# Kernel optimization log

Hardware: AMD Instinct MI355X
Metric: run time of the kernel (lower is better)

## Reference

```python
import jax, jax.numpy as jnp
import numpy as np

N_NODES = 100000
N_EDGES = 1600000
IN_DIM = 128
HID = 128
OUT = 64


def gcn_conv(x, src, dst, W, b, n_nodes):
    # x: [N, Din] -> [N, Dout]; symmetric-normalized GCN with self-loops (PyG GCNConv defaults)
    h = x @ W  # transform first (as PyG does)
    loop = jnp.arange(n_nodes, dtype=src.dtype)
    s = jnp.concatenate([src, loop])
    d = jnp.concatenate([dst, loop])
    deg = jax.ops.segment_sum(jnp.ones_like(d, dtype=h.dtype), d, num_segments=n_nodes)
    dis = jnp.where(deg > 0, jax.lax.rsqrt(deg), 0.0)
    norm = dis[s] * dis[d]  # [E+N]
    msgs = h[s] * norm[:, None]  # gather-transform
    out = jax.ops.segment_sum(msgs, d, num_segments=n_nodes)  # scatter-add
    return out + b


def setup_inputs() -> dict:
    key = jax.random.key(0)
    ks = jax.random.split(key, 12)
    x = jax.random.normal(ks[0], (N_NODES, IN_DIM), dtype=jnp.float32)
    edge_index = jax.random.randint(ks[1], (2, N_EDGES), 0, N_NODES, dtype=jnp.int32)
    def lin(k, fan_in, fan_out):
        bound = 1.0 / np.sqrt(fan_in)
        kw, kb = jax.random.split(k)
        W = jax.random.uniform(kw, (fan_in, fan_out), minval=-bound, maxval=bound, dtype=jnp.float32)
        b = jax.random.uniform(kb, (fan_out,), minval=-bound, maxval=bound, dtype=jnp.float32)
        return W, b
    W1, b1 = lin(ks[2], IN_DIM, HID)
    W2, b2 = lin(ks[3], HID, HID)
    Wp1, bp1 = lin(ks[4], HID, HID)
    Wp2, bp2 = lin(ks[5], HID, OUT)
    return {"x": x, "edge_index": edge_index,
            "W1": W1, "b1": b1, "W2": W2, "b2": b2,
            "Wp1": Wp1, "bp1": bp1, "Wp2": Wp2, "bp2": bp2}


def reference(x, edge_index, W1, b1, W2, b2, Wp1, bp1, Wp2, bp2):
    n = x.shape[0]
    src, dst = edge_index[0], edge_index[1]
    # layer 1: GCNConv + relu (dropout inactive at eval)
    h = jax.nn.relu(gcn_conv(x, src, dst, W1, b1, n))
    # layer 2
    h = jax.nn.relu(gcn_conv(h, src, dst, W2, b2, n))
    # post MLP head
    h = h @ Wp1 + bp1
    h = h @ Wp2 + bp2
    return jax.nn.log_softmax(h, axis=1)
```

## Files before the change

kernel.cpp:

```cpp
#include <hip/hip_runtime.h>
#include <hip/hip_bf16.h>
#include <cstdint>

typedef __attribute__((ext_vector_type(8))) short short8;
typedef __attribute__((ext_vector_type(16))) float f32x16;
typedef unsigned short us;

#define BIN_SHIFT 9
#define BIN_NODES 512
#define CAPB 12288
#define EPB 4096

__device__ __forceinline__ float bflo(uint32_t u) { return __builtin_bit_cast(float, u << 16); }
__device__ __forceinline__ float bfhi(uint32_t u) { return __builtin_bit_cast(float, u & 0xffff0000u); }

__device__ __forceinline__ us f32_to_bf16_rne(float f) {
  uint32_t u = __builtin_bit_cast(uint32_t, f);
  u += 0x7fffu + ((u >> 16) & 1u);
  return (us)(u >> 16);
}

__device__ __forceinline__ void split2(float f, us& h, us& l) {
  uint32_t u = __builtin_bit_cast(uint32_t, f);
  h = (us)(u >> 16);
  float fh = __builtin_bit_cast(float, u & 0xffff0000u);
  float r = f - fh;
  l = (us)(__builtin_bit_cast(uint32_t, r) >> 16);
}

__global__ __launch_bounds__(256) void k_binA(
    const int* __restrict__ src, const int* __restrict__ dst,
    uint2* __restrict__ binbuf, int* __restrict__ gcur, int E, int nbins) {
  __shared__ uint2 stage[EPB];
  __shared__ int cnt[256], base[256], cur[256], gbase[256];
  int tid = threadIdx.x;
  int e0 = blockIdx.x * EPB;
  int ne = min(EPB, E - e0);
  if (ne <= 0) return;
  cnt[tid] = 0;
  __syncthreads();
  for (int i = tid; i < ne; i += 256) atomicAdd(&cnt[dst[e0 + i] >> BIN_SHIFT], 1);
  __syncthreads();
  if (tid < 64) {
    int carry = 0;
#pragma unroll
    for (int c = 0; c < 4; ++c) {
      int v = cnt[c * 64 + tid];
      int incl = v;
#pragma unroll
      for (int off = 1; off < 64; off <<= 1) {
        int t = __shfl_up(incl, off, 64);
        if (tid >= off) incl += t;
      }
      base[c * 64 + tid] = carry + incl - v;
      carry += __shfl(incl, 63, 64);
    }
  }
  __syncthreads();
  if (tid < nbins && cnt[tid] > 0) gbase[tid] = atomicAdd(&gcur[tid], cnt[tid]);
  cur[tid] = base[tid];
  __syncthreads();
  for (int i = tid; i < ne; i += 256) {
    int d = dst[e0 + i], s = src[e0 + i];
    int p = atomicAdd(&cur[d >> BIN_SHIFT], 1);
    stage[p] = make_uint2((unsigned)d, (unsigned)s);
  }
  __syncthreads();
  for (int i = tid; i < ne; i += 256) {
    uint2 en = stage[i];
    int b = en.x >> BIN_SHIFT;
    int gi = gbase[b] + (i - base[b]);
    if (gi < CAPB) binbuf[(size_t)b * CAPB + gi] = en;
  }
}

__global__ __launch_bounds__(256) void k_passB(
    const uint2* __restrict__ binbuf, const int* __restrict__ gcur,
    int* __restrict__ deg, float* __restrict__ dis, int* __restrict__ start,
    int* __restrict__ col, int N, int nbins) {
  __shared__ int hist[512], lstart[512], cur[512];
  __shared__ int colstage[CAPB];
  __shared__ int binbase_s;
  int b = blockIdx.x, tid = threadIdx.x;
  int node0 = b << BIN_SHIFT;
  int cnt = min(gcur[b], CAPB);
  hist[tid] = 0; hist[tid + 256] = 0;
  __syncthreads();
  const uint2* bp = binbuf + (size_t)b * CAPB;
  for (int i = tid; i < cnt; i += 256) atomicAdd(&hist[bp[i].x & (BIN_NODES - 1)], 1);
  __syncthreads();
  if (tid < 64) {
    int s = 0;
    for (int i = tid; i < b; i += 64) s += min(gcur[i], CAPB);
#pragma unroll
    for (int off = 32; off; off >>= 1) s += __shfl_xor(s, off, 64);
    if (tid == 0) binbase_s = s;
    int carry = 0;
#pragma unroll
    for (int c = 0; c < 8; ++c) {
      int v = hist[c * 64 + tid];
      int incl = v;
#pragma unroll
      for (int off = 1; off < 64; off <<= 1) {
        int t = __shfl_up(incl, off, 64);
        if (tid >= off) incl += t;
      }
      lstart[c * 64 + tid] = carry + incl - v;
      carry += __shfl(incl, 63, 64);
    }
  }
  __syncthreads();
  int binbase = binbase_s;
  for (int i = tid; i < 512; i += 256) {
    int node = node0 + i;
    if (node < N) {
      int dg = hist[i];
      deg[node] = dg;
      dis[node] = rsqrtf((float)(dg + 1));
      start[node] = binbase + lstart[i];
    }
  }
  cur[tid] = lstart[tid]; cur[tid + 256] = lstart[tid + 256];
  __syncthreads();
  for (int i = tid; i < cnt; i += 256) {
    uint2 en = bp[i];
    int p = atomicAdd(&cur[en.x & (BIN_NODES - 1)], 1);
    colstage[p] = (int)en.y;
  }
  __syncthreads();
  for (int i = tid; i < cnt; i += 256) col[binbase + i] = colstage[i];
}

__global__ void k_prep(const float* __restrict__ W1, const float* __restrict__ W2,
                       const float* __restrict__ Wp1, const float* __restrict__ Wp2,
                       const float* __restrict__ bp1, const float* __restrict__ bp2,
                       us* __restrict__ Wt1h, us* __restrict__ Wt1l,
                       us* __restrict__ Wt2h, us* __restrict__ Wt2l,
                       us* __restrict__ Wch, us* __restrict__ Wcl, float* __restrict__ bc) {
  int blk = blockIdx.x, tid = threadIdx.x;
  if (blk < 128) {
    const float* W = (blk < 64) ? W1 : W2;
    us* Wh = (blk < 64) ? Wt1h : Wt2h;
    us* Wl = (blk < 64) ? Wt1l : Wt2l;
    int idx = (blk & 63) * 256 + tid;
    int k = idx >> 7, n = idx & 127;
    us h, l;
    split2(W[idx], h, l);
    Wh[n * 128 + k] = h;
    Wl[n * 128 + k] = l;
  } else if (blk < 160) {
    int idx = (blk - 128) * 256 + tid;
    int k = idx >> 6, j = idx & 63;
    float acc = 0.f;
    for (int t = 0; t < 128; ++t) acc += Wp1[k * 128 + t] * Wp2[t * 64 + j];
    us h, l;
    split2(acc, h, l);
    Wch[j * 128 + k] = h;
    Wcl[j * 128 + k] = l;
  } else {
    int j = tid;
    if (j < 64) {
      float acc = bp2[j];
      for (int t = 0; t < 128; ++t) acc += bp1[t] * Wp2[t * 64 + j];
      bc[j] = acc;
    }
  }
}

template <bool AF32>
__global__ __launch_bounds__(256) void k_gemm_mfma(
    const void* __restrict__ Av, const us* __restrict__ Wh,
    const us* __restrict__ Wl, const float* __restrict__ dis,
    us* __restrict__ out_bf16, int N, int ntiles) {
  __shared__ us As_hi[32 * 136];
  __shared__ us As_lo[32 * 136];
  int tid = threadIdx.x;
  int wave = tid >> 6, lane = tid & 63;
  int n0 = wave * 32;
  int nn = n0 + (lane & 31);
  int khalf = (lane >> 5) * 8;
  int m = lane & 31;

  short8 bh[8], bl[8];
#pragma unroll
  for (int c = 0; c < 8; ++c) {
    bh[c] = *(const short8*)&Wh[nn * 128 + c * 16 + khalf];
    bl[c] = *(const short8*)&Wl[nn * 128 + c * 16 + khalf];
  }

  for (int t = blockIdx.x; t < ntiles; t += gridDim.x) {
    int row0 = t * 32;
    __syncthreads();
    if (AF32) {
      const float* A = (const float*)Av;
      for (int j = tid; j < 1024; j += 256) {
        int r = j >> 5, c = j & 31;
        int row = row0 + r;
        float4 v = make_float4(0.f, 0.f, 0.f, 0.f);
        if (row < N) v = *(const float4*)&A[(size_t)row * 128 + c * 4];
        us h0, h1, h2, h3, l0, l1, l2, l3;
        split2(v.x, h0, l0); split2(v.y, h1, l1);
        split2(v.z, h2, l2); split2(v.w, h3, l3);
        *(ushort4*)&As_hi[r * 136 + c * 4] = make_ushort4(h0, h1, h2, h3);
        *(ushort4*)&As_lo[r * 136 + c * 4] = make_ushort4(l0, l1, l2, l3);
      }
    } else {
      const us* A = (const us*)Av;
      for (int j = tid; j < 512; j += 256) {
        int r = j >> 4, c = j & 15;
        int row = row0 + r;
        uint4 v = make_uint4(0u, 0u, 0u, 0u);
        if (row < N) v = *(const uint4*)&A[(size_t)row * 128 + c * 8];
        *(uint4*)&As_hi[r * 136 + c * 8] = v;
      }
    }
    __syncthreads();

    f32x16 acc = {};
#pragma unroll
    for (int c = 0; c < 8; ++c) {
      short8 ah = *(const short8*)&As_hi[m * 136 + c * 16 + khalf];
      acc = __builtin_amdgcn_mfma_f32_32x32x16_bf16(ah, bh[c], acc, 0, 0, 0);
      acc = __builtin_amdgcn_mfma_f32_32x32x16_bf16(ah, bl[c], acc, 0, 0, 0);
      if (AF32) {
        short8 al = *(const short8*)&As_lo[m * 136 + c * 16 + khalf];
        acc = __builtin_amdgcn_mfma_f32_32x32x16_bf16(al, bh[c], acc, 0, 0, 0);
      }
    }

    int col = n0 + (lane & 31);
    int rbase = row0 + 4 * (lane >> 5);
#pragma unroll
    for (int reg = 0; reg < 16; ++reg) {
      int row = rbase + (reg & 3) + 8 * (reg >> 2);
      if (row < N) {
        float v = acc[reg] * dis[row];
        out_bf16[(size_t)row * 128 + col] = f32_to_bf16_rne(v);
      }
    }
  }
}

__global__ __launch_bounds__(256) void k_gather(
    const us* __restrict__ h, us* __restrict__ o,
    const int* __restrict__ start, const int* __restrict__ deg,
    const int* __restrict__ col, const float* __restrict__ dis,
    const float* __restrict__ bias, int N) {
  int tid = threadIdx.x;
  int node = blockIdx.x * 8 + (tid >> 5);
  int lane = tid & 31;
  if (node >= N) return;
  const uint2* h2 = (const uint2*)h;
  uint2 u = h2[(size_t)node * 32 + lane];
  float ax = bflo(u.x), ay = bfhi(u.x), az = bflo(u.y), aw = bfhi(u.y);
  int e = start[node];
  int e_end = e + deg[node];
  for (; e + 1 < e_end; e += 2) {
    uint2 u1 = h2[(size_t)col[e] * 32 + lane];
    uint2 u2 = h2[(size_t)col[e + 1] * 32 + lane];
    ax += bflo(u1.x) + bflo(u2.x); ay += bfhi(u1.x) + bfhi(u2.x);
    az += bflo(u1.y) + bflo(u2.y); aw += bfhi(u1.y) + bfhi(u2.y);
  }
  if (e < e_end) {
    uint2 u1 = h2[(size_t)col[e] * 32 + lane];
    ax += bflo(u1.x); ay += bfhi(u1.x); az += bflo(u1.y); aw += bfhi(u1.y);
  }
  float sc = dis[node];
  float4 b = ((const float4*)bias)[lane];
  float rx = fmaxf(ax * sc + b.x, 0.f);
  float ry = fmaxf(ay * sc + b.y, 0.f);
  float rz = fmaxf(az * sc + b.z, 0.f);
  float rw = fmaxf(aw * sc + b.w, 0.f);
  uint2 po;
  po.x = ((uint32_t)f32_to_bf16_rne(ry) << 16) | f32_to_bf16_rne(rx);
  po.y = ((uint32_t)f32_to_bf16_rne(rw) << 16) | f32_to_bf16_rne(rz);
  ((uint2*)o)[(size_t)node * 32 + lane] = po;
}

__global__ __launch_bounds__(256) void k_head_mfma(
    const us* __restrict__ act, const us* __restrict__ Wch,
    const us* __restrict__ Wcl, const float* __restrict__ bc,
    float* __restrict__ out, int N) {
  __shared__ us As[64 * 136];
  __shared__ float red[2][2][64];
  int tid = threadIdx.x;
  int wave = tid >> 6, lane = tid & 63;
  int rt = wave >> 1, ct = wave & 1;
  int colj = ct * 32 + (lane & 31);
  int khalf = (lane >> 5) * 8;
  int m = lane & 31;

  short8 bh[8], bl[8];
#pragma unroll
  for (int c = 0; c < 8; ++c) {
    bh[c] = *(const short8*)&Wch[colj * 128 + c * 16 + khalf];
    bl[c] = *(const short8*)&Wcl[colj * 128 + c * 16 + khalf];
  }

  int row0 = blockIdx.x * 64;
  for (int j = tid; j < 1024; j += 256) {
    int r = j >> 4, c = j & 15;
    int row = row0 + r;
    uint4 v = make_uint4(0u, 0u, 0u, 0u);
    if (row < N) v = *(const uint4*)&act[(size_t)row * 128 + c * 8];
    *(uint4*)&As[r * 136 + c * 8] = v;
  }
  __syncthreads();

  f32x16 acc = {};
  int mrow = rt * 32 + m;
#pragma unroll
  for (int c = 0; c < 8; ++c) {
    short8 ah = *(const short8*)&As[mrow * 136 + c * 16 + khalf];
    acc = __builtin_amdgcn_mfma_f32_32x32x16_bf16(ah, bh[c], acc, 0, 0, 0);
    acc = __builtin_amdgcn_mfma_f32_32x32x16_bf16(ah, bl[c], acc, 0, 0, 0);
  }

  float bcv = bc[colj];
  float lg[16], mx[16];
#pragma unroll
  for (int reg = 0; reg < 16; ++reg) {
    lg[reg] = acc[reg] + bcv;
    float v = lg[reg];
#pragma unroll
    for (int off = 16; off > 0; off >>= 1) v = fmaxf(v, __shfl_xor(v, off, 32));
    mx[reg] = v;
  }
  if ((lane & 31) == 0) {
#pragma unroll
    for (int reg = 0; reg < 16; ++reg) {
      int rl = rt * 32 + (reg & 3) + 8 * (reg >> 2) + 4 * (lane >> 5);
      red[0][ct][rl] = mx[reg];
    }
  }
  __syncthreads();

  float ex[16], sm[16];
#pragma unroll
  for (int reg = 0; reg < 16; ++reg) {
    int rl = rt * 32 + (reg & 3) + 8 * (reg >> 2) + 4 * (lane >> 5);
    float rmax = fmaxf(red[0][0][rl], red[0][1][rl]);
    ex[reg] = lg[reg] - rmax;
    float v = expf(ex[reg]);
#pragma unroll
    for (int off = 16; off > 0; off >>= 1) v += __shfl_xor(v, off, 32);
    sm[reg] = v;
  }
  if ((lane & 31) == 0) {
#pragma unroll
    for (int reg = 0; reg < 16; ++reg) {
      int rl = rt * 32 + (reg & 3) + 8 * (reg >> 2) + 4 * (lane >> 5);
      red[1][ct][rl] = sm[reg];
    }
  }
  __syncthreads();

#pragma unroll
  for (int reg = 0; reg < 16; ++reg) {
    int rl = rt * 32 + (reg & 3) + 8 * (reg >> 2) + 4 * (lane >> 5);
    int row = row0 + rl;
    if (row < N) {
      float total = red[1][0][rl] + red[1][1][rl];
      out[(size_t)row * 64 + colj] = ex[reg] - logf(total);
    }
  }
}

extern "C" void kernel_launch(void* const* d_in, const int* in_sizes, int n_in,
                              void* d_out, int out_size, void* d_ws, size_t ws_size,
                              hipStream_t stream) {
  const float* x   = (const float*)d_in[0];
  const int*   ei  = (const int*)d_in[1];
  const float* W1  = (const float*)d_in[2];
  const float* b1  = (const float*)d_in[3];
  const float* W2  = (const float*)d_in[4];
  const float* b2  = (const float*)d_in[5];
  const float* Wp1 = (const float*)d_in[6];
  const float* bp1 = (const float*)d_in[7];
  const float* Wp2 = (const float*)d_in[8];
  const float* bp2 = (const float*)d_in[9];
  float* out = (float*)d_out;

  int N = in_sizes[0] / 128;
  int E = in_sizes[1] / 2;
  const int* src = ei;
  const int* dst = ei + E;
  int nbins = (N + BIN_NODES - 1) >> BIN_SHIFT;

  float* dis   = (float*)d_ws;
  int*   deg   = (int*)(dis + N);
  int*   start = deg + N;
  int*   col   = start + N;
  int*   gcur  = col + ((E + 3) & ~3);
  us* Wt1h = (us*)(gcur + 256);
  us* Wt1l = Wt1h + 16384;
  us* Wt2h = Wt1l + 16384;
  us* Wt2l = Wt2h + 16384;
  us* Wch  = Wt2l + 16384;
  us* Wcl  = Wch + 8192;
  float* bc = (float*)(Wcl + 8192);
  uint2* binbuf = (uint2*)(bc + 80);
  us* hbuf = (us*)(binbuf + (size_t)nbins * CAPB);
  us* act  = hbuf + (size_t)N * 128;

  hipMemsetAsync(gcur, 0, 256 * sizeof(int), stream);

  int ablocks = (E + EPB - 1) / EPB;
  k_binA<<<ablocks, 256, 0, stream>>>(src, dst, binbuf, gcur, E, nbins);
  k_passB<<<nbins, 256, 0, stream>>>(binbuf, gcur, deg, dis, start, col, N, nbins);
  k_prep<<<161, 256, 0, stream>>>(W1, W2, Wp1, Wp2, bp1, bp2,
                                  Wt1h, Wt1l, Wt2h, Wt2l, Wch, Wcl, bc);

  int ntiles = (N + 31) / 32;
  int gemm_grid = ntiles < 1024 ? ntiles : 1024;
  int agblocks = (N + 7) / 8;
  int hblocks = (N + 63) / 64;

  k_gemm_mfma<true><<<gemm_grid, 256, 0, stream>>>(x, Wt1h, Wt1l, dis, hbuf, N, ntiles);
  k_gather<<<agblocks, 256, 0, stream>>>(hbuf, act, start, deg, col, dis, b1, N);
  k_gemm_mfma<false><<<gemm_grid, 256, 0, stream>>>(act, Wt2h, Wt2l, dis, hbuf, N, ntiles);
  k_gather<<<agblocks, 256, 0, stream>>>(hbuf, act, start, deg, col, dis, b2, N);
  k_head_mfma<<<hblocks, 256, 0, stream>>>(act, Wch, Wcl, bc, out, N);
}
```

Measured before the change: 409.3 us.

## Pack bin entries into 32-bit words, widen gather loads, launch one GEMM tile per block

```diff
diff --git a/kernel.cpp b/kernel.cpp
--- a/kernel.cpp
+++ b/kernel.cpp
@@ -30,8 +30,8 @@
 
 __global__ __launch_bounds__(256) void k_binA(
     const int* __restrict__ src, const int* __restrict__ dst,
-    uint2* __restrict__ binbuf, int* __restrict__ gcur, int E, int nbins) {
-  __shared__ uint2 stage[EPB];
+    uint32_t* __restrict__ binbuf, int* __restrict__ gcur, int E, int nbins) {
+  __shared__ uint32_t stage[EPB];
   __shared__ int cnt[256], base[256], cur[256], gbase[256];
   int tid = threadIdx.x;
   int e0 = blockIdx.x * EPB;
@@ -63,19 +63,24 @@
   for (int i = tid; i < ne; i += 256) {
     int d = dst[e0 + i], s = src[e0 + i];
     int p = atomicAdd(&cur[d >> BIN_SHIFT], 1);
-    stage[p] = make_uint2((unsigned)d, (unsigned)s);
+    stage[p] = ((uint32_t)(d & (BIN_NODES - 1)) << 23) | (uint32_t)s;
   }
   __syncthreads();
   for (int i = tid; i < ne; i += 256) {
-    uint2 en = stage[i];
-    int b = en.x >> BIN_SHIFT;
+    uint32_t en = stage[i];
+    int lo = 0, hi = 255;
+    while (lo < hi) {
+      int mid = (lo + hi + 1) >> 1;
+      if (base[mid] <= i) lo = mid; else hi = mid - 1;
+    }
+    int b = lo;
     int gi = gbase[b] + (i - base[b]);
     if (gi < CAPB) binbuf[(size_t)b * CAPB + gi] = en;
   }
 }
 
 __global__ __launch_bounds__(256) void k_passB(
-    const uint2* __restrict__ binbuf, const int* __restrict__ gcur,
+    const uint32_t* __restrict__ binbuf, const int* __restrict__ gcur,
     int* __restrict__ deg, float* __restrict__ dis, int* __restrict__ start,
     int* __restrict__ col, int N, int nbins) {
   __shared__ int hist[512], lstart[512], cur[512];
@@ -86,8 +91,8 @@
   int cnt = min(gcur[b], CAPB);
   hist[tid] = 0; hist[tid + 256] = 0;
   __syncthreads();
-  const uint2* bp = binbuf + (size_t)b * CAPB;
-  for (int i = tid; i < cnt; i += 256) atomicAdd(&hist[bp[i].x & (BIN_NODES - 1)], 1);
+  const uint32_t* bp = binbuf + (size_t)b * CAPB;
+  for (int i = tid; i < cnt; i += 256) atomicAdd(&hist[bp[i] >> 23], 1);
   __syncthreads();
   if (tid < 64) {
     int s = 0;
@@ -123,9 +128,9 @@
   cur[tid] = lstart[tid]; cur[tid + 256] = lstart[tid + 256];
   __syncthreads();
   for (int i = tid; i < cnt; i += 256) {
-    uint2 en = bp[i];
-    int p = atomicAdd(&cur[en.x & (BIN_NODES - 1)], 1);
-    colstage[p] = (int)en.y;
+    uint32_t en = bp[i];
+    int p = atomicAdd(&cur[en >> 23], 1);
+    colstage[p] = (int)(en & 0x7fffffu);
   }
   __syncthreads();
   for (int i = tid; i < cnt; i += 256) col[binbase + i] = colstage[i];
@@ -171,7 +176,7 @@
 __global__ __launch_bounds__(256) void k_gemm_mfma(
     const void* __restrict__ Av, const us* __restrict__ Wh,
     const us* __restrict__ Wl, const float* __restrict__ dis,
-    us* __restrict__ out_bf16, int N, int ntiles) {
+    us* __restrict__ out_bf16, int N) {
   __shared__ us As_hi[32 * 136];
   __shared__ us As_lo[32 * 136];
   int tid = threadIdx.x;
@@ -188,55 +193,52 @@
     bl[c] = *(const short8*)&Wl[nn * 128 + c * 16 + khalf];
   }
 
-  for (int t = blockIdx.x; t < ntiles; t += gridDim.x) {
-    int row0 = t * 32;
-    __syncthreads();
+  int row0 = blockIdx.x * 32;
+  if (AF32) {
+    const float* A = (const float*)Av;
+    for (int j = tid; j < 1024; j += 256) {
+      int r = j >> 5, c = j & 31;
+      int row = row0 + r;
+      float4 v = make_float4(0.f, 0.f, 0.f, 0.f);
+      if (row < N) v = *(const float4*)&A[(size_t)row * 128 + c * 4];
+      us h0, h1, h2, h3, l0, l1, l2, l3;
+      split2(v.x, h0, l0); split2(v.y, h1, l1);
+      split2(v.z, h2, l2); split2(v.w, h3, l3);
+      *(ushort4*)&As_hi[r * 136 + c * 4] = make_ushort4(h0, h1, h2, h3);
+      *(ushort4*)&As_lo[r * 136 + c * 4] = make_ushort4(l0, l1, l2, l3);
+    }
+  } else {
+    const us* A = (const us*)Av;
+    for (int j = tid; j < 512; j += 256) {
+      int r = j >> 4, c = j & 15;
+      int row = row0 + r;
+      uint4 v = make_uint4(0u, 0u, 0u, 0u);
+      if (row < N) v = *(const uint4*)&A[(size_t)row * 128 + c * 8];
+      *(uint4*)&As_hi[r * 136 + c * 8] = v;
+    }
+  }
+  __syncthreads();
+
+  f32x16 acc = {};
+#pragma unroll
+  for (int c = 0; c < 8; ++c) {
+    short8 ah = *(const short8*)&As_hi[m * 136 + c * 16 + khalf];
+    acc = __builtin_amdgcn_mfma_f32_32x32x16_bf16(ah, bh[c], acc, 0, 0, 0);
+    acc = __builtin_amdgcn_mfma_f32_32x32x16_bf16(ah, bl[c], acc, 0, 0, 0);
     if (AF32) {
-      const float* A = (const float*)Av;
-      for (int j = tid; j < 1024; j += 256) {
-        int r = j >> 5, c = j & 31;
-        int row = row0 + r;
-        float4 v = make_float4(0.f, 0.f, 0.f, 0.f);
-        if (row < N) v = *(const float4*)&A[(size_t)row * 128 + c * 4];
-        us h0, h1, h2, h3, l0, l1, l2, l3;
-        split2(v.x, h0, l0); split2(v.y, h1, l1);
-        split2(v.z, h2, l2); split2(v.w, h3, l3);
-        *(ushort4*)&As_hi[r * 136 + c * 4] = make_ushort4(h0, h1, h2, h3);
-        *(ushort4*)&As_lo[r * 136 + c * 4] = make_ushort4(l0, l1, l2, l3);
-      }
-    } else {
-      const us* A = (const us*)Av;
-      for (int j = tid; j < 512; j += 256) {
-        int r = j >> 4, c = j & 15;
-        int row = row0 + r;
-        uint4 v = make_uint4(0u, 0u, 0u, 0u);
-        if (row < N) v = *(const uint4*)&A[(size_t)row * 128 + c * 8];
-        *(uint4*)&As_hi[r * 136 + c * 8] = v;
-      }
-    }
-    __syncthreads();
-
-    f32x16 acc = {};
-#pragma unroll
-    for (int c = 0; c < 8; ++c) {
-      short8 ah = *(const short8*)&As_hi[m * 136 + c * 16 + khalf];
-      acc = __builtin_amdgcn_mfma_f32_32x32x16_bf16(ah, bh[c], acc, 0, 0, 0);
-      acc = __builtin_amdgcn_mfma_f32_32x32x16_bf16(ah, bl[c], acc, 0, 0, 0);
-      if (AF32) {
-        short8 al = *(const short8*)&As_lo[m * 136 + c * 16 + khalf];
-        acc = __builtin_amdgcn_mfma_f32_32x32x16_bf16(al, bh[c], acc, 0, 0, 0);
-      }
-    }
-
-    int col = n0 + (lane & 31);
-    int rbase = row0 + 4 * (lane >> 5);
-#pragma unroll
-    for (int reg = 0; reg < 16; ++reg) {
-      int row = rbase + (reg & 3) + 8 * (reg >> 2);
-      if (row < N) {
-        float v = acc[reg] * dis[row];
-        out_bf16[(size_t)row * 128 + col] = f32_to_bf16_rne(v);
-      }
+      short8 al = *(const short8*)&As_lo[m * 136 + c * 16 + khalf];
+      acc = __builtin_amdgcn_mfma_f32_32x32x16_bf16(al, bh[c], acc, 0, 0, 0);
+    }
+  }
+
+  int colj = n0 + (lane & 31);
+  int rbase = row0 + 4 * (lane >> 5);
+#pragma unroll
+  for (int reg = 0; reg < 16; ++reg) {
+    int row = rbase + (reg & 3) + 8 * (reg >> 2);
+    if (row < N) {
+      float v = acc[reg] * dis[row];
+      out_bf16[(size_t)row * 128 + colj] = f32_to_bf16_rne(v);
     }
   }
 }
@@ -247,34 +249,48 @@
     const int* __restrict__ col, const float* __restrict__ dis,
     const float* __restrict__ bias, int N) {
   int tid = threadIdx.x;
-  int node = blockIdx.x * 8 + (tid >> 5);
-  int lane = tid & 31;
+  int node = blockIdx.x * 16 + (tid >> 4);
+  int ln = tid & 15;
   if (node >= N) return;
-  const uint2* h2 = (const uint2*)h;
-  uint2 u = h2[(size_t)node * 32 + lane];
-  float ax = bflo(u.x), ay = bfhi(u.x), az = bflo(u.y), aw = bfhi(u.y);
+  const uint4* h4 = (const uint4*)h;
+  uint4 u = h4[(size_t)node * 16 + ln];
+  float a0 = bflo(u.x), a1 = bfhi(u.x), a2 = bflo(u.y), a3 = bfhi(u.y);
+  float a4 = bflo(u.z), a5 = bfhi(u.z), a6 = bflo(u.w), a7 = bfhi(u.w);
   int e = start[node];
   int e_end = e + deg[node];
-  for (; e + 1 < e_end; e += 2) {
-    uint2 u1 = h2[(size_t)col[e] * 32 + lane];
-    uint2 u2 = h2[(size_t)col[e + 1] * 32 + lane];
-    ax += bflo(u1.x) + bflo(u2.x); ay += bfhi(u1.x) + bfhi(u2.x);
-    az += bflo(u1.y) + bflo(u2.y); aw += bfhi(u1.y) + bfhi(u2.y);
-  }
-  if (e < e_end) {
-    uint2 u1 = h2[(size_t)col[e] * 32 + lane];
-    ax += bflo(u1.x); ay += bfhi(u1.x); az += bflo(u1.y); aw += bfhi(u1.y);
+  for (; e + 3 < e_end; e += 4) {
+    int s0 = col[e], s1 = col[e + 1], s2 = col[e + 2], s3 = col[e + 3];
+    uint4 v0 = h4[(size_t)s0 * 16 + ln];
+    uint4 v1 = h4[(size_t)s1 * 16 + ln];
+    uint4 v2 = h4[(size_t)s2 * 16 + ln];
+    uint4 v3 = h4[(size_t)s3 * 16 + ln];
+    a0 += (bflo(v0.x) + bflo(v1.x)) + (bflo(v2.x) + bflo(v3.x));
+    a1 += (bfhi(v0.x) + bfhi(v1.x)) + (bfhi(v2.x) + bfhi(v3.x));
+    a2 += (bflo(v0.y) + bflo(v1.y)) + (bflo(v2.y) + bflo(v3.y));
+    a3 += (bfhi(v0.y) + bfhi(v1.y)) + (bfhi(v2.y) + bfhi(v3.y));
+    a4 += (bflo(v0.z) + bflo(v1.z)) + (bflo(v2.z) + bflo(v3.z));
+    a5 += (bfhi(v0.z) + bfhi(v1.z)) + (bfhi(v2.z) + bfhi(v3.z));
+    a6 += (bflo(v0.w) + bflo(v1.w)) + (bflo(v2.w) + bflo(v3.w));
+    a7 += (bfhi(v0.w) + bfhi(v1.w)) + (bfhi(v2.w) + bfhi(v3.w));
+  }
+  for (; e < e_end; ++e) {
+    uint4 v0 = h4[(size_t)col[e] * 16 + ln];
+    a0 += bflo(v0.x); a1 += bfhi(v0.x); a2 += bflo(v0.y); a3 += bfhi(v0.y);
+    a4 += bflo(v0.z); a5 += bfhi(v0.z); a6 += bflo(v0.w); a7 += bfhi(v0.w);
   }
   float sc = dis[node];
-  float4 b = ((const float4*)bias)[lane];
-  float rx = fmaxf(ax * sc + b.x, 0.f);
-  float ry = fmaxf(ay * sc + b.y, 0.f);
-  float rz = fmaxf(az * sc + b.z, 0.f);
-  float rw = fmaxf(aw * sc + b.w, 0.f);
-  uint2 po;
-  po.x = ((uint32_t)f32_to_bf16_rne(ry) << 16) | f32_to_bf16_rne(rx);
-  po.y = ((uint32_t)f32_to_bf16_rne(rw) << 16) | f32_to_bf16_rne(rz);
-  ((uint2*)o)[(size_t)node * 32 + lane] = po;
+  float4 b0 = ((const float4*)bias)[ln * 2];
+  float4 b1 = ((const float4*)bias)[ln * 2 + 1];
+  float r0 = fmaxf(a0 * sc + b0.x, 0.f), r1 = fmaxf(a1 * sc + b0.y, 0.f);
+  float r2 = fmaxf(a2 * sc + b0.z, 0.f), r3 = fmaxf(a3 * sc + b0.w, 0.f);
+  float r4 = fmaxf(a4 * sc + b1.x, 0.f), r5 = fmaxf(a5 * sc + b1.y, 0.f);
+  float r6 = fmaxf(a6 * sc + b1.z, 0.f), r7 = fmaxf(a7 * sc + b1.w, 0.f);
+  uint4 po;
+  po.x = ((uint32_t)f32_to_bf16_rne(r1) << 16) | f32_to_bf16_rne(r0);
+  po.y = ((uint32_t)f32_to_bf16_rne(r3) << 16) | f32_to_bf16_rne(r2);
+  po.z = ((uint32_t)f32_to_bf16_rne(r5) << 16) | f32_to_bf16_rne(r4);
+  po.w = ((uint32_t)f32_to_bf16_rne(r7) << 16) | f32_to_bf16_rne(r6);
+  ((uint4*)o)[(size_t)node * 16 + ln] = po;
 }
 
 __global__ __launch_bounds__(256) void k_head_mfma(
@@ -399,7 +415,7 @@
   us* Wch  = Wt2l + 16384;
   us* Wcl  = Wch + 8192;
   float* bc = (float*)(Wcl + 8192);
-  uint2* binbuf = (uint2*)(bc + 80);
+  uint32_t* binbuf = (uint32_t*)(bc + 80);
   us* hbuf = (us*)(binbuf + (size_t)nbins * CAPB);
   us* act  = hbuf + (size_t)N * 128;
 
@@ -412,13 +428,12 @@
                                   Wt1h, Wt1l, Wt2h, Wt2l, Wch, Wcl, bc);
 
   int ntiles = (N + 31) / 32;
-  int gemm_grid = ntiles < 1024 ? ntiles : 1024;
-  int agblocks = (N + 7) / 8;
+  int agblocks = (N + 15) / 16;
   int hblocks = (N + 63) / 64;
 
-  k_gemm_mfma<true><<<gemm_grid, 256, 0, stream>>>(x, Wt1h, Wt1l, dis, hbuf, N, ntiles);
+  k_gemm_mfma<true><<<ntiles, 256, 0, stream>>>(x, Wt1h, Wt1l, dis, hbuf, N);
   k_gather<<<agblocks, 256, 0, stream>>>(hbuf, act, start, deg, col, dis, b1, N);
-  k_gemm_mfma<false><<<gemm_grid, 256, 0, stream>>>(act, Wt2h, Wt2l, dis, hbuf, N, ntiles);
+  k_gemm_mfma<false><<<ntiles, 256, 0, stream>>>(act, Wt2h, Wt2l, dis, hbuf, N);
   k_gather<<<agblocks, 256, 0, stream>>>(hbuf, act, start, deg, col, dis, b2, N);
   k_head_mfma<<<hblocks, 256, 0, stream>>>(act, Wch, Wcl, bc, out, N);
 }
```

Result: slower. 429.2 us (+4.9%).
